# Performance work log

Measured on AMD Instinct MI355X. Metric: run time of the kernel, lower is better.

The kernel has to match this reference:

```python
import jax, jax.numpy as jnp
import numpy as np

N, C, NBINS = 4096, 32000, 15


def setup_inputs() -> dict:
    key = jax.random.key(0)
    k1, k2, k3 = jax.random.split(key, 3)
    inp = jax.random.normal(k1, (N, C), dtype=jnp.float32)
    target = jax.random.randint(k2, (N,), 0, C, dtype=jnp.int32)
    # contiguous calibration bins over [0, 1]: upper bounds sorted ascending
    bin_uppers = jnp.arange(1, NBINS + 1, dtype=jnp.float32) / NBINS
    # per-bin gamma_next_epoch values
    bin_gammas = jax.random.uniform(k3, (NBINS,), dtype=jnp.float32, minval=0.5, maxval=5.0)
    return {"input": inp, "target": target, "bin_uppers": bin_uppers, "bin_gammas": bin_gammas}


def reference(input, target, bin_uppers, bin_gammas):
    # log_softmax over classes, gather true-class log-prob
    logp = jax.nn.log_softmax(input, axis=1)                     # [N, C]
    probs = jnp.exp(logp)                                        # softmax_logits [N, C]
    logp_k = jnp.take_along_axis(logp, target[:, None].astype(jnp.int32), axis=1)[:, 0]  # [N]
    p_k = jnp.exp(logp_k)                                        # [N]
    # p_j = largest prob strictly below p_k (top-1 of masked probs; 0 if none)
    p_j = jnp.max(jnp.where(probs < p_k[:, None], probs, 0.0), axis=1)  # [N]
    pt = p_k - p_j
    # vectorized bin search replacing the serial per-sample loop:
    # first bin with pt < upper_bound, clipped so pt >= last upper -> last bin
    idx = jnp.clip(jnp.searchsorted(bin_uppers, pt, side='right'), 0, NBINS - 1)
    gamma = bin_gammas[idx]                                      # [N]
    loss = -((1.0 - p_k + p_j) ** gamma) * logp_k                # [N]
    return jnp.sum(loss)  # size_average=False
```

## Files before the change

### kernel.cpp

```cpp
#include <hip/hip_runtime.h>
#include <math.h>

#define NBINS 15
#define BLK 256

__global__ __launch_bounds__(BLK) void row_loss_kernel(
    const float* __restrict__ inp,
    const int* __restrict__ target,
    const float* __restrict__ uppers,
    const float* __restrict__ gammas,
    float* __restrict__ row_loss,
    int C)
{
    const int row = blockIdx.x;
    const float* __restrict__ x = inp + (size_t)row * (size_t)C;
    const float xt = x[target[row]];

    float m  = -INFINITY;
    float s  = 0.0f;
    float m2 = -INFINITY;

    const int nvec = C >> 2;
    const float4* __restrict__ xv = (const float4*)x;

    for (int i = threadIdx.x; i < nvec; i += BLK) {
        float4 v = xv[i];
        float f;
        f = v.x; if (f > m) { s *= __expf(m - f); m = f; } s += __expf(f - m); if (f < xt) m2 = fmaxf(m2, f);
        f = v.y; if (f > m) { s *= __expf(m - f); m = f; } s += __expf(f - m); if (f < xt) m2 = fmaxf(m2, f);
        f = v.z; if (f > m) { s *= __expf(m - f); m = f; } s += __expf(f - m); if (f < xt) m2 = fmaxf(m2, f);
        f = v.w; if (f > m) { s *= __expf(m - f); m = f; } s += __expf(f - m); if (f < xt) m2 = fmaxf(m2, f);
    }
    for (int i = (nvec << 2) + threadIdx.x; i < C; i += BLK) {
        float f = x[i];
        if (f > m) { s *= __expf(m - f); m = f; }
        s += __expf(f - m);
        if (f < xt) m2 = fmaxf(m2, f);
    }

    #pragma unroll
    for (int off = 32; off > 0; off >>= 1) {
        float om  = __shfl_xor(m,  off);
        float os  = __shfl_xor(s,  off);
        float om2 = __shfl_xor(m2, off);
        float M = fmaxf(m, om);
        s = s * __expf(m - M) + os * __expf(om - M);
        m = M;
        m2 = fmaxf(m2, om2);
    }

    __shared__ float sm[4], ss[4], sm2[4];
    const int wid  = threadIdx.x >> 6;
    const int lane = threadIdx.x & 63;
    if (lane == 0) { sm[wid] = m; ss[wid] = s; sm2[wid] = m2; }
    __syncthreads();

    if (threadIdx.x == 0) {
        m = sm[0]; s = ss[0]; m2 = sm2[0];
        #pragma unroll
        for (int w = 1; w < 4; ++w) {
            float M = fmaxf(m, sm[w]);
            s = s * __expf(m - M) + ss[w] * __expf(sm[w] - M);
            m = M;
            m2 = fmaxf(m2, sm2[w]);
        }
        const float logZ  = m + __logf(s);
        const float logpk = xt - logZ;
        const float pk    = __expf(logpk);
        const float pj    = (m2 == -INFINITY) ? 0.0f : __expf(m2 - logZ);
        const float pt    = pk - pj;

        int idx = 0;
        #pragma unroll
        for (int j = 0; j < NBINS; ++j) idx += (uppers[j] <= pt) ? 1 : 0;
        if (idx > NBINS - 1) idx = NBINS - 1;

        const float gamma = gammas[idx];
        const float base  = 1.0f - pk + pj;
        row_loss[row] = -__powf(base, gamma) * logpk;
    }
}

__global__ __launch_bounds__(BLK) void sum_kernel(
    const float* __restrict__ v, float* __restrict__ out, int n)
{
    float acc = 0.0f;
    for (int i = threadIdx.x; i < n; i += BLK) acc += v[i];
    #pragma unroll
    for (int off = 32; off > 0; off >>= 1) acc += __shfl_xor(acc, off);
    __shared__ float sacc[4];
    const int wid  = threadIdx.x >> 6;
    const int lane = threadIdx.x & 63;
    if (lane == 0) sacc[wid] = acc;
    __syncthreads();
    if (threadIdx.x == 0) out[0] = sacc[0] + sacc[1] + sacc[2] + sacc[3];
}

extern "C" void kernel_launch(void* const* d_in, const int* in_sizes, int n_in,
                              void* d_out, int out_size, void* d_ws, size_t ws_size,
                              hipStream_t stream) {
    const float* inp    = (const float*)d_in[0];
    const int*   target = (const int*)d_in[1];
    const float* uppers = (const float*)d_in[2];
    const float* gammas = (const float*)d_in[3];
    float* out = (float*)d_out;
    float* ws  = (float*)d_ws;

    const int N = in_sizes[1];
    const int C = in_sizes[0] / N;

    row_loss_kernel<<<N, BLK, 0, stream>>>(inp, target, uppers, gammas, ws, C);
    sum_kernel<<<1, BLK, 0, stream>>>(ws, out, N);
}
```

Measured before the change: 105.1 us.

## Fuse final sum via last-block atomic counter; dual accumulators with nontemporal loads

```diff
diff --git a/kernel.cpp b/kernel.cpp
--- a/kernel.cpp
+++ b/kernel.cpp
@@ -3,6 +3,21 @@
 
 #define NBINS 15
 #define BLK 256
+
+typedef float v4f __attribute__((ext_vector_type(4)));
+
+#define PROC4(v, k)                                                              \
+    do {                                                                         \
+        float f;                                                                 \
+        f = (v).x; if (f > m##k) { s##k *= __expf(m##k - f); m##k = f; }         \
+        s##k += __expf(f - m##k); if (f < xt) m2##k = fmaxf(m2##k, f);           \
+        f = (v).y; if (f > m##k) { s##k *= __expf(m##k - f); m##k = f; }         \
+        s##k += __expf(f - m##k); if (f < xt) m2##k = fmaxf(m2##k, f);           \
+        f = (v).z; if (f > m##k) { s##k *= __expf(m##k - f); m##k = f; }         \
+        s##k += __expf(f - m##k); if (f < xt) m2##k = fmaxf(m2##k, f);           \
+        f = (v).w; if (f > m##k) { s##k *= __expf(m##k - f); m##k = f; }         \
+        s##k += __expf(f - m##k); if (f < xt) m2##k = fmaxf(m2##k, f);           \
+    } while (0)
 
 __global__ __launch_bounds__(BLK) void row_loss_kernel(
     const float* __restrict__ inp,
@@ -10,53 +25,65 @@
     const float* __restrict__ uppers,
     const float* __restrict__ gammas,
     float* __restrict__ row_loss,
-    int C)
+    unsigned int* __restrict__ counter,
+    float* __restrict__ out,
+    int C, int N)
 {
     const int row = blockIdx.x;
     const float* __restrict__ x = inp + (size_t)row * (size_t)C;
     const float xt = x[target[row]];
 
-    float m  = -INFINITY;
-    float s  = 0.0f;
-    float m2 = -INFINITY;
+    float m0 = -INFINITY, s0 = 0.0f, m20 = -INFINITY;
+    float m1 = -INFINITY, s1 = 0.0f, m21 = -INFINITY;
 
     const int nvec = C >> 2;
-    const float4* __restrict__ xv = (const float4*)x;
+    const v4f* __restrict__ xv = (const v4f*)x;
 
-    for (int i = threadIdx.x; i < nvec; i += BLK) {
-        float4 v = xv[i];
-        float f;
-        f = v.x; if (f > m) { s *= __expf(m - f); m = f; } s += __expf(f - m); if (f < xt) m2 = fmaxf(m2, f);
-        f = v.y; if (f > m) { s *= __expf(m - f); m = f; } s += __expf(f - m); if (f < xt) m2 = fmaxf(m2, f);
-        f = v.z; if (f > m) { s *= __expf(m - f); m = f; } s += __expf(f - m); if (f < xt) m2 = fmaxf(m2, f);
-        f = v.w; if (f > m) { s *= __expf(m - f); m = f; } s += __expf(f - m); if (f < xt) m2 = fmaxf(m2, f);
+    int i = threadIdx.x;
+    for (; i + BLK < nvec; i += 2 * BLK) {
+        v4f a = __builtin_nontemporal_load(&xv[i]);
+        v4f b = __builtin_nontemporal_load(&xv[i + BLK]);
+        PROC4(a, 0);
+        PROC4(b, 1);
     }
-    for (int i = (nvec << 2) + threadIdx.x; i < C; i += BLK) {
-        float f = x[i];
-        if (f > m) { s *= __expf(m - f); m = f; }
-        s += __expf(f - m);
-        if (f < xt) m2 = fmaxf(m2, f);
+    if (i < nvec) {
+        v4f a = __builtin_nontemporal_load(&xv[i]);
+        PROC4(a, 0);
+    }
+    for (int j = (nvec << 2) + threadIdx.x; j < C; j += BLK) {
+        float f = x[j];
+        if (f > m0) { s0 *= __expf(m0 - f); m0 = f; }
+        s0 += __expf(f - m0);
+        if (f < xt) m20 = fmaxf(m20, f);
+    }
+
+    {
+        float M = fmaxf(m0, m1);
+        s0 = s0 * __expf(m0 - M) + s1 * __expf(m1 - M);
+        m0 = M;
+        m20 = fmaxf(m20, m21);
     }
 
     #pragma unroll
     for (int off = 32; off > 0; off >>= 1) {
-        float om  = __shfl_xor(m,  off);
-        float os  = __shfl_xor(s,  off);
-        float om2 = __shfl_xor(m2, off);
-        float M = fmaxf(m, om);
-        s = s * __expf(m - M) + os * __expf(om - M);
-        m = M;
-        m2 = fmaxf(m2, om2);
+        float om  = __shfl_xor(m0,  off);
+        float os  = __shfl_xor(s0,  off);
+        float om2 = __shfl_xor(m20, off);
+        float M = fmaxf(m0, om);
+        s0 = s0 * __expf(m0 - M) + os * __expf(om - M);
+        m0 = M;
+        m20 = fmaxf(m20, om2);
     }
 
     __shared__ float sm[4], ss[4], sm2[4];
+    __shared__ bool amLast;
     const int wid  = threadIdx.x >> 6;
     const int lane = threadIdx.x & 63;
-    if (lane == 0) { sm[wid] = m; ss[wid] = s; sm2[wid] = m2; }
+    if (lane == 0) { sm[wid] = m0; ss[wid] = s0; sm2[wid] = m20; }
     __syncthreads();
 
     if (threadIdx.x == 0) {
-        m = sm[0]; s = ss[0]; m2 = sm2[0];
+        float m = sm[0], s = ss[0], m2 = sm2[0];
         #pragma unroll
         for (int w = 1; w < 4; ++w) {
             float M = fmaxf(m, sm[w]);
@@ -78,22 +105,24 @@
         const float gamma = gammas[idx];
         const float base  = 1.0f - pk + pj;
         row_loss[row] = -__powf(base, gamma) * logpk;
+
+        __threadfence();
+        unsigned int t = atomicAdd(counter, 1u);
+        amLast = (t == (unsigned int)(gridDim.x - 1));
     }
-}
+    __syncthreads();
 
-__global__ __launch_bounds__(BLK) void sum_kernel(
-    const float* __restrict__ v, float* __restrict__ out, int n)
-{
-    float acc = 0.0f;
-    for (int i = threadIdx.x; i < n; i += BLK) acc += v[i];
-    #pragma unroll
-    for (int off = 32; off > 0; off >>= 1) acc += __shfl_xor(acc, off);
-    __shared__ float sacc[4];
-    const int wid  = threadIdx.x >> 6;
-    const int lane = threadIdx.x & 63;
-    if (lane == 0) sacc[wid] = acc;
-    __syncthreads();
-    if (threadIdx.x == 0) out[0] = sacc[0] + sacc[1] + sacc[2] + sacc[3];
+    if (amLast) {
+        __threadfence();
+        float acc = 0.0f;
+        for (int j = threadIdx.x; j < N; j += BLK) acc += row_loss[j];
+        #pragma unroll
+        for (int off = 32; off > 0; off >>= 1) acc += __shfl_xor(acc, off);
+        __shared__ float sacc[4];
+        if (lane == 0) sacc[wid] = acc;
+        __syncthreads();
+        if (threadIdx.x == 0) out[0] = sacc[0] + sacc[1] + sacc[2] + sacc[3];
+    }
 }
 
 extern "C" void kernel_launch(void* const* d_in, const int* in_sizes, int n_in,
@@ -104,11 +133,15 @@
     const float* uppers = (const float*)d_in[2];
     const float* gammas = (const float*)d_in[3];
     float* out = (float*)d_out;
-    float* ws  = (float*)d_ws;
 
     const int N = in_sizes[1];
     const int C = in_sizes[0] / N;
 
-    row_loss_kernel<<<N, BLK, 0, stream>>>(inp, target, uppers, gammas, ws, C);
-    sum_kernel<<<1, BLK, 0, stream>>>(ws, out, N);
+    float* row_loss = (float*)d_ws;
+    const size_t counter_off = ((size_t)N * sizeof(float) + 127) & ~(size_t)127;
+    unsigned int* counter = (unsigned int*)((char*)d_ws + counter_off);
+
+    (void)hipMemsetAsync(counter, 0, sizeof(unsigned int), stream);
+    row_loss_kernel<<<N, BLK, 0, stream>>>(inp, target, uppers, gammas,
+                                           row_loss, counter, out, C, N);
 }
```

New measurement: 290.3 us. 176% more time.
